# Kernel tuning notes

Hardware: AMD Instinct MI355X
Metric: run time of the kernel (lower is better)

## Reference

```python
import jax, jax.numpy as jnp
import numpy as np

B = 2
IMG = (128, 256, 256)
P = 16
E, NH, DH = 768, 12, 64
L, F = 12, 3072
WS = (512, 1024, 2048)   # LongNet segment lengths
RS = (1, 2, 4)           # matching dilation ratios
NEG = -1e9
NPATCH = (IMG[0] // P) * (IMG[1] // P) * (IMG[2] // P)
S = NPATCH + 1           # +1 CLS token


def setup_inputs() -> dict:
    key = jax.random.key(0)
    ks = jax.random.split(key, 16)
    def nrm(k, shape, std=0.02):
        return jax.random.normal(k, shape, jnp.float32) * std
    return {
        "x": jax.random.normal(ks[0], (B, 1) + IMG, jnp.float32),
        "conv_w": nrm(ks[1], (E, 1, P, P, P)),
        "conv_b": jnp.zeros((E,), jnp.float32),
        "cls_token": nrm(ks[2], (1, 1, E)),
        "pos_embed": nrm(ks[3], (1, S, E)),
        "ln1_g": jnp.ones((L, E)), "ln1_b": jnp.zeros((L, E)),
        "wq": nrm(ks[4], (L, E, E)), "bq": jnp.zeros((L, E)),
        "wk": nrm(ks[5], (L, E, E)), "bk": jnp.zeros((L, E)),
        "wv": nrm(ks[6], (L, E, E)), "bv": jnp.zeros((L, E)),
        "wo": nrm(ks[7], (L, E, E)), "bo": jnp.zeros((L, E)),
        "ln2_g": jnp.ones((L, E)), "ln2_b": jnp.zeros((L, E)),
        "w1": nrm(ks[8], (L, E, F)), "b1": jnp.zeros((L, F)),
        "w2": nrm(ks[9], (L, F, E)), "b2": jnp.zeros((L, E)),
        "normf_g": jnp.ones((E,)), "normf_b": jnp.zeros((E,)),
    }


def _ln(x, g, b, eps=1e-5):
    m = x.mean(-1, keepdims=True)
    v = ((x - m) ** 2).mean(-1, keepdims=True)
    return (x - m) * jax.lax.rsqrt(v + eps) * g + b


def _dilated_branch(q, k, v, w, r):
    # LongNet dilated attention for one (segment_length w, dilation r) config.
    # q,k,v: [B,S,H,d]. Head h uses offset h % r inside each segment of length w.
    b, s0, h, d = q.shape
    sp = -(-s0 // w) * w
    pad = sp - s0
    qp, kp, vp = (jnp.pad(t, ((0, 0), (0, pad), (0, 0), (0, 0))) for t in (q, k, v))
    n, m = sp // w, w // r
    idx = (jnp.arange(h)[:, None] % r) + jnp.arange(m)[None, :] * r      # [h,m]
    seg = lambda t: t.reshape(b, n, w, h, d).transpose(0, 1, 3, 2, 4)    # [b,n,h,w,d]
    gidx = idx[None, None, :, :, None]
    qs = jnp.take_along_axis(seg(qp), gidx, axis=3)                      # [b,n,h,m,d]
    ks = jnp.take_along_axis(seg(kp), gidx, axis=3)
    vs = jnp.take_along_axis(seg(vp), gidx, axis=3)
    kvalid = (jnp.arange(sp) < s0).reshape(n, w)[:, idx]                 # [n,h,m]
    scores = jnp.einsum('bnhqd,bnhkd->bnhqk', qs, ks) * (d ** -0.5)
    scores = jnp.where(kvalid[None, :, :, None, :], scores, NEG)
    lse = jax.nn.logsumexp(scores, axis=-1)                              # [b,n,h,m]
    out = jnp.einsum('bnhqk,bnhkd->bnhqd', jax.nn.softmax(scores, -1), vs)
    hh = jnp.arange(h)[:, None]
    out_f = jnp.zeros((b, n, h, w, d), q.dtype).at[:, :, hh, idx, :].set(out)
    lse_f = jnp.full((b, n, h, w), NEG, q.dtype).at[:, :, hh, idx].set(lse)
    return (out_f.transpose(0, 1, 3, 2, 4).reshape(b, sp, h, d),
            lse_f.transpose(0, 1, 3, 2).reshape(b, sp, h))


def _dilated_attention(q, k, v):
    # Combine branches weighted by softmax normalizers (exp lse), per LongNet.
    b, s0, h, d = q.shape
    smax = max(-(-s0 // w) * w for w in WS)
    outs, lses = [], []
    for w, r in zip(WS, RS):
        o, l = _dilated_branch(q, k, v, w, r)
        outs.append(jnp.pad(o, ((0, 0), (0, smax - o.shape[1]), (0, 0), (0, 0))))
        lses.append(jnp.pad(l, ((0, 0), (0, smax - l.shape[1]), (0, 0)),
                            constant_values=NEG))
    wgt = jax.nn.softmax(jnp.stack(lses), axis=0)[..., None]             # [nb,b,smax,h,1]
    out = (wgt * jnp.stack(outs)).sum(0)                                 # [b,smax,h,d]
    return out[:, :s0]


def reference(x, conv_w, conv_b, cls_token, pos_embed, ln1_g, ln1_b, wq, bq,
              wk, bk, wv, bv, wo, bo, ln2_g, ln2_b, w1, b1, w2, b2,
              normf_g, normf_b):
    b = x.shape[0]
    dp, hp, wp = IMG[0] // P, IMG[1] // P, IMG[2] // P
    # Conv3d patch embed with stride == kernel -> block reshape + matmul
    xp = x.reshape(b, 1, dp, P, hp, P, wp, P).transpose(0, 2, 4, 6, 1, 3, 5, 7)
    xp = xp.reshape(b, dp * hp * wp, -1) @ conv_w.reshape(E, -1).T + conv_b
    h = jnp.concatenate([jnp.broadcast_to(cls_token, (b, 1, E)), xp], axis=1)
    h = h + pos_embed  # seq length matches pos_embed, no interpolation needed

    def layer(hst, p):
        g1, lb1, Wq, Bq, Wk, Bk, Wv, Bv, Wo, Bo, g2, lb2, W1, B1, W2, B2 = p
        y = _ln(hst, g1, lb1)
        q = (y @ Wq + Bq).reshape(b, S, NH, DH)
        k = (y @ Wk + Bk).reshape(b, S, NH, DH)
        v = (y @ Wv + Bv).reshape(b, S, NH, DH)
        a = _dilated_attention(q, k, v).reshape(b, S, E) @ Wo + Bo
        hst = hst + a
        y = _ln(hst, g2, lb2)
        hst = hst + jax.nn.gelu(y @ W1 + B1, approximate=False) @ W2 + B2
        return hst, None

    params = (ln1_g, ln1_b, wq, bq, wk, bk, wv, bv, wo, bo,
              ln2_g, ln2_b, w1, b1, w2, b2)
    h, _ = jax.lax.scan(layer, h, params)
    h = _ln(h, normf_g, normf_b)
    return h[:, 0]
```

## Files before the change

kernel.cpp:

```cpp
#include <hip/hip_runtime.h>
#include <math.h>

#define SEQ 2049
#define EMB 768
#define NHEADS 12
#define QKVW 2304
#define MROWS 4098
#define MPAD 4224
#define NEGV -1000000000.0f

typedef short bs8 __attribute__((ext_vector_type(8)));
typedef float f4 __attribute__((ext_vector_type(4)));

__device__ __forceinline__ unsigned short f2bf(float f){
  union { float f; unsigned u; } x; x.f = f;
  unsigned r = x.u + 0x7fffu + ((x.u >> 16) & 1u);
  return (unsigned short)(r >> 16);
}
__device__ __forceinline__ unsigned short f2bf_fast(float f){
  union { float f; unsigned u; } x; x.f = f;
  return (unsigned short)((x.u + 0x8000u) >> 16);
}
__device__ __forceinline__ float bf2f(unsigned short u){
  union { unsigned u; float f; } x; x.u = ((unsigned)u) << 16; return x.f;
}

__device__ __forceinline__ float gelu_f(float x){
  float ax = fabsf(x)*0.70710678f;
  float t = 1.f/(1.f + 0.3275911f*ax);
  float p = t*(0.254829592f + t*(-0.284496736f + t*(1.421413741f
            + t*(-1.453152027f + t*1.061405429f))));
  float erfv = 1.f - p*__expf(-ax*ax);
  float s = (x >= 0.f) ? erfv : -erfv;
  return 0.5f*x*(1.f + s);
}

__device__ __forceinline__ void gl_lds16(const void* g, void* l){
  __builtin_amdgcn_global_load_lds((const __attribute__((address_space(1))) void*)g,
                                   (__attribute__((address_space(3))) void*)l, 16, 0, 0);
}

__global__ void wtr_k(const float* __restrict__ src, unsigned short* __restrict__ dst,
                      int K, int N, int LD, int NOFF)
{
  __shared__ float tile[32][33];
  int k0 = blockIdx.x*32, n0 = blockIdx.y*32, z = blockIdx.z;
  int tx = threadIdx.x, ty = threadIdx.y;
  const float* s = src + (size_t)z*K*N;
#pragma unroll
  for (int i=0;i<4;++i)
    tile[ty*4+i][tx] = s[(size_t)(k0+ty*4+i)*N + n0+tx];
  __syncthreads();
  unsigned short* dz = dst + ((size_t)z*LD + NOFF)*K;
#pragma unroll
  for (int i=0;i<4;++i)
    dz[(size_t)(n0+ty*4+i)*K + k0+tx] = f2bf(tile[tx][ty*4+i]);
}

__global__ void castconv_k(const float* __restrict__ src, unsigned short* __restrict__ dst){
  size_t i = ((size_t)blockIdx.x*256 + threadIdx.x)*4;
  float4 f = *(const float4*)(src+i);
  dst[i+0]=f2bf(f.x); dst[i+1]=f2bf(f.y); dst[i+2]=f2bf(f.z); dst[i+3]=f2bf(f.w);
}

__global__ void biascat_k(const float* __restrict__ bq, const float* __restrict__ bk,
                          const float* __restrict__ bv, float* __restrict__ dst){
  int i = blockIdx.x*256+threadIdx.x;
  int l = i/QKVW, c = i%QKVW;
  float v = (c<768) ? bq[l*768+c] : (c<1536 ? bk[l*768+c-768] : bv[l*768+c-1536]);
  dst[i] = v;
}

__global__ void patchify_k(const float* __restrict__ x, unsigned short* __restrict__ Xp)
{
  size_t gid = (size_t)blockIdx.x*256 + threadIdx.x;
  size_t oi = gid*4;
  int row = (int)(oi >> 12);
  int c = (int)(oi & 4095);
  int b = row >> 11; int p = row & 2047;
  int pd = p >> 8, ph = (p>>4)&15, pw = p&15;
  int pz = c >> 8, py = (c>>4)&15, px = c&15;
  size_t src = (((size_t)(b*128 + pd*16+pz)*256) + (size_t)(ph*16+py))*256 + (size_t)(pw*16+px);
  float4 f = *(const float4*)(x+src);
  Xp[oi+0]=f2bf(f.x); Xp[oi+1]=f2bf(f.y); Xp[oi+2]=f2bf(f.z); Xp[oi+3]=f2bf(f.w);
}

__global__ void assemble_k(const float* __restrict__ P, size_t pstride,
                           const float* __restrict__ cls,
                           const float* __restrict__ pos_e, float* __restrict__ H)
{
  int row = blockIdx.x; int t = threadIdx.x;
  float* hr = H + (size_t)row*EMB;
  if (row >= MROWS) { hr[t]=0.f; hr[t+256]=0.f; hr[t+512]=0.f; return; }
  int b = row / SEQ; int pos = row - b*SEQ;
#pragma unroll
  for (int c0=0;c0<3;++c0) {
    int c = t + c0*256;
    float v;
    if (pos==0) v = cls[c];
    else {
      size_t idx = ((size_t)(b*2048 + pos-1))*EMB + c;
      v = P[idx] + P[pstride+idx] + P[2*pstride+idx] + P[3*pstride+idx];
    }
    hr[c] = v + pos_e[(size_t)pos*EMB + c];
  }
}

__global__ __launch_bounds__(256) void ln_k(const float* __restrict__ H,
    const float* __restrict__ gam, const float* __restrict__ bet,
    unsigned short* __restrict__ Y)
{
  int row = blockIdx.x, t = threadIdx.x;
  const float* hr = H + (size_t)row*EMB;
  float v0 = hr[t], v1 = hr[t+256], v2 = hr[t+512];
  float s = v0+v1+v2;
#pragma unroll
  for (int off=32; off>=1; off>>=1) s += __shfl_down(s, off);
  __shared__ float r1[4], r2[4];
  if ((t&63)==0) r1[t>>6] = s;
  __syncthreads();
  float mean = (r1[0]+r1[1]+r1[2]+r1[3]) * (1.f/768.f);
  float d0=v0-mean, d1=v1-mean, d2=v2-mean;
  float q = d0*d0+d1*d1+d2*d2;
#pragma unroll
  for (int off=32; off>=1; off>>=1) q += __shfl_down(q, off);
  if ((t&63)==0) r2[t>>6] = q;
  __syncthreads();
  float rstd = rsqrtf((r2[0]+r2[1]+r2[2]+r2[3])*(1.f/768.f) + 1e-5f);
  unsigned short* yr = Y + (size_t)row*EMB;
  yr[t]     = f2bf(d0*rstd*gam[t]     + bet[t]);
  yr[t+256] = f2bf(d1*rstd*gam[t+256] + bet[t+256]);
  yr[t+512] = f2bf(d2*rstd*gam[t+512] + bet[t+512]);
}

template<int S>
__global__ __launch_bounds__(256) void ln_red_k(float* __restrict__ H,
    const float* __restrict__ P, size_t pstride,
    const float* __restrict__ gam, const float* __restrict__ bet,
    unsigned short* __restrict__ Y)
{
  int row = blockIdx.x, t = threadIdx.x;
  size_t base = (size_t)row*EMB;
  float v[3];
#pragma unroll
  for (int c0=0;c0<3;++c0) {
    size_t idx = base + t + c0*256;
    float h = H[idx];
#pragma unroll
    for (int s=0;s<S;++s) h += P[(size_t)s*pstride + idx];
    H[idx] = h; v[c0] = h;
  }
  float s = v[0]+v[1]+v[2];
#pragma unroll
  for (int off=32; off>=1; off>>=1) s += __shfl_down(s, off);
  __shared__ float r1[4], r2[4];
  if ((t&63)==0) r1[t>>6] = s;
  __syncthreads();
  float mean = (r1[0]+r1[1]+r1[2]+r1[3]) * (1.f/768.f);
  float d0=v[0]-mean, d1=v[1]-mean, d2=v[2]-mean;
  float q = d0*d0+d1*d1+d2*d2;
#pragma unroll
  for (int off=32; off>=1; off>>=1) q += __shfl_down(q, off);
  if ((t&63)==0) r2[t>>6] = q;
  __syncthreads();
  float rstd = rsqrtf((r2[0]+r2[1]+r2[2]+r2[3])*(1.f/768.f) + 1e-5f);
  unsigned short* yr = Y + base;
  yr[t]     = f2bf(d0*rstd*gam[t]     + bet[t]);
  yr[t+256] = f2bf(d1*rstd*gam[t+256] + bet[t+256]);
  yr[t+512] = f2bf(d2*rstd*gam[t+512] + bet[t+512]);
}

template<int S>
__global__ __launch_bounds__(256) void final_ln_red_k(const float* __restrict__ H,
   const float* __restrict__ P, size_t pstride,
   const float* __restrict__ gam, const float* __restrict__ bet, float* __restrict__ out)
{
  int b = blockIdx.x, t = threadIdx.x;
  size_t base = (size_t)(b*SEQ)*EMB;
  float v[3];
#pragma unroll
  for (int c0=0;c0<3;++c0) {
    size_t idx = base + t + c0*256;
    float h = H[idx];
#pragma unroll
    for (int s=0;s<S;++s) h += P[(size_t)s*pstride + idx];
    v[c0] = h;
  }
  float s = v[0]+v[1]+v[2];
#pragma unroll
  for (int off=32; off>=1; off>>=1) s += __shfl_down(s, off);
  __shared__ float r1[4], r2[4];
  if ((t&63)==0) r1[t>>6] = s;
  __syncthreads();
  float mean = (r1[0]+r1[1]+r1[2]+r1[3]) * (1.f/768.f);
  float d0=v[0]-mean, d1=v[1]-mean, d2=v[2]-mean;
  float q = d0*d0+d1*d1+d2*d2;
#pragma unroll
  for (int off=32; off>=1; off>>=1) q += __shfl_down(q, off);
  if ((t&63)==0) r2[t>>6] = q;
  __syncthreads();
  float rstd = rsqrtf((r2[0]+r2[1]+r2[2]+r2[3])*(1.f/768.f) + 1e-5f);
  out[b*EMB + t]     = d0*rstd*gam[t]     + bet[t];
  out[b*EMB + t+256] = d1*rstd*gam[t+256] + bet[t+256];
  out[b*EMB + t+512] = d2*rstd*gam[t+512] + bet[t+512];
}

template<int MODE, int NSPLIT>
__global__ __launch_bounds__(512) void gemm_k(
    const unsigned short* __restrict__ A,
    const unsigned short* __restrict__ Bt,
    const float* __restrict__ bias,
    unsigned short* __restrict__ Cb,
    float* __restrict__ Cf,
    int K, int ldc, size_t splitStride)
{
  __shared__ __attribute__((aligned(16))) unsigned short lA[3][128*32];
  __shared__ __attribute__((aligned(16))) unsigned short lB[3][128*32];
  const int tid = threadIdx.x;
  const int w = tid>>6, lane = tid&63, g = lane>>4, l16 = lane&15;
  const int lr = lane>>2;
  const int lcs = (((lane&3) ^ ((lane>>3)&3)))*8;
  const int swz = ((g ^ ((l16>>1)&3)))*8;
  const int nwg = gridDim.x*gridDim.y;
  const int id = blockIdx.y*gridDim.x + blockIdx.x;
  const int q = nwg>>3, r = nwg&7, xc = id&7, si = id>>3;
  const int nid = (xc<r ? xc*(q+1) : r*(q+1)+(xc-r)*q) + si;
  const int tm = nid / gridDim.x;
  const int tn = nid - tm*gridDim.x;
  const int kchunk = K / NSPLIT;
  const int kofs = (NSPLIT>1) ? blockIdx.z * kchunk : 0;
  const unsigned short* Ab = A + (size_t)tm*128*K + kofs;
  const unsigned short* Bb = Bt + (size_t)tn*128*K + kofs;
  const int wm = (w>>2)*64, wn = (w&3)*32;
  f4 acc[4][2] = {};
  const int nkt = kchunk>>5;

  auto STAGE = [&](int buf, int kt){
    const size_t ko = (size_t)(kt*32 + lcs);
    gl_lds16(Ab + (size_t)(w*16 + lr)*K + ko, ((char*)lA[buf]) + w*1024);
    gl_lds16(Bb + (size_t)(w*16 + lr)*K + ko, ((char*)lB[buf]) + w*1024);
  };

  STAGE(0, 0);
  STAGE(1, 1);
  for (int kt=0; kt<nkt; ++kt) {
    const int cur = kt % 3;
    if (kt+2 < nkt) {
      STAGE((kt+2)%3, kt+2);
      asm volatile("s_waitcnt vmcnt(4)" ::: "memory");
    } else if (kt+1 < nkt) {
      asm volatile("s_waitcnt vmcnt(2)" ::: "memory");
    } else {
      asm volatile("s_waitcnt vmcnt(0)" ::: "memory");
    }
    __builtin_amdgcn_sched_barrier(0);
    __builtin_amdgcn_s_barrier();
    bs8 af[4], bf[2];
#pragma unroll
    for (int mi=0;mi<4;++mi) af[mi] = *(const bs8*)(lA[cur] + (wm+mi*16+l16)*32 + swz);
#pragma unroll
    for (int ni=0;ni<2;++ni) bf[ni] = *(const bs8*)(lB[cur] + (wn+ni*16+l16)*32 + swz);
    asm volatile("s_waitcnt lgkmcnt(0)" ::: "memory");
    __builtin_amdgcn_sched_barrier(0);
    __builtin_amdgcn_s_barrier();
#pragma unroll
    for (int mi=0;mi<4;++mi)
#pragma unroll
      for (int ni=0;ni<2;++ni)
        acc[mi][ni] = __builtin_amdgcn_mfma_f32_16x16x32_bf16(af[mi], bf[ni], acc[mi][ni], 0,0,0);
  }
  const float bscale = (NSPLIT==1 || blockIdx.z==0) ? 1.f : 0.f;
#pragma unroll
  for (int mi=0;mi<4;++mi)
#pragma unroll
    for (int ni=0;ni<2;++ni) {
      int col = tn*128 + wn + ni*16 + l16;
      float bv = bias[col]*bscale;
#pragma unroll
      for (int r0=0;r0<4;++r0) {
        int row = tm*128 + wm + mi*16 + g*4 + r0;
        float val = acc[mi][ni][r0] + bv;
        if (MODE==1) val = gelu_f(val);
        if (MODE<=1) Cb[(size_t)row*ldc + col] = f2bf(val);
        else Cf[(size_t)blockIdx.z*splitStride + (size_t)row*ldc + col] = val;
      }
    }
}

__global__ __launch_bounds__(256) void attn_all_k(
    const unsigned short* __restrict__ qkv,
    unsigned short* __restrict__ O1, float* __restrict__ L1,
    unsigned short* __restrict__ O2, float* __restrict__ L2,
    unsigned short* __restrict__ O3, float* __restrict__ L3)
{
  __shared__ __attribute__((aligned(16))) unsigned short lsm[128*72 + 64*136];
  unsigned short* lK  = lsm;
  unsigned short* lVt = lsm + 128*72;
  const int tid = threadIdx.x;
  const int w = tid>>6, lane = tid&63, g = lane>>4, l16 = lane&15;

  int id = (blockIdx.x & 7)*240 + (blockIdx.x >> 3);
  int R, WSZ, NSEG; unsigned short* OB; float* LB;
  if (id < 960)       { R=1; WSZ=512;  NSEG=5; OB=O1; LB=L1; }
  else if (id < 1536) { id -= 960;  R=2; WSZ=1024; NSEG=3; OB=O2; LB=L2; }
  else                { id -= 1536; R=4; WSZ=2048; NSEG=2; OB=O3; LB=L3; }
  const int qt = id & 7; int rest = id >> 3;
  const int seg = rest % NSEG; const int bh = rest / NSEG;
  const int b = bh / NHEADS, hd = bh % NHEADS;
  const int hr = hd % R;
  const int kbase = seg*WSZ + hr;
  bs8 z = {0,0,0,0,0,0,0,0};

  if (kbase + qt*64*R >= SEQ) {
    size_t ob2 = ((size_t)(b*NSEG + seg)*NHEADS + hd)*512 + qt*64;
    int row = tid>>2, cb = (tid&3)*16;
    *(bs8*)(&OB[(ob2 + row)*64 + cb])     = z;
    *(bs8*)(&OB[(ob2 + row)*64 + cb + 8]) = z;
    if (tid < 64) LB[ob2 + tid] = NEGV;
    return;
  }
  int nvk = (SEQ - 1 - kbase)/R + 1; if (nvk > 512) nvk = 512;
  const int nck = (nvk + 127) >> 7;

  const int j0 = qt*64 + w*16;
  const unsigned short* qkvb = qkv + (size_t)b*SEQ*QKVW;

  bs8 qf0 = z, qf1 = z;
  {
    int qpos = kbase + (j0 + l16)*R;
    if (qpos < SEQ) {
      const unsigned short* qrow = qkvb + (size_t)qpos*QKVW + hd*64 + g*8;
      qf0 = *(const bs8*)(qrow);
      qf1 = *(const bs8*)(qrow + 32);
    }
  }

  const int dbK = tid&7, kkKb = tid>>3;
  const int kkV = tid&127, dbV0 = tid>>7;
  const unsigned short* pK = qkvb + (size_t)(kbase + kkKb*R)*QKVW + EMB + hd*64 + dbK*8;
  const unsigned short* pV = qkvb + (size_t)(kbase + kkV*R)*QKVW + 1536 + hd*64 + dbV0*8;
  const size_t stepIt = (size_t)32*R*QKVW;
  const size_t stepC  = (size_t)128*R*QKVW;
  int ci = 0;
  bs8 kreg[4], vreg[4];
  auto ISSUE = [&](){
    const bool full = (kbase + (ci*128 + 127)*R) < SEQ;
    if (full) {
#pragma unroll
      for (int it=0; it<4; ++it) kreg[it] = *(const bs8*)(pK + (size_t)it*stepIt);
#pragma unroll
      for (int it=0; it<4; ++it) vreg[it] = *(const bs8*)(pV + it*16);
    } else {
      const int cofs = ci*128*R;
#pragma unroll
      for (int it=0; it<4; ++it)
        kreg[it] = (kbase + (kkKb + it*32)*R + cofs < SEQ)
                   ? *(const bs8*)(pK + (size_t)it*stepIt) : z;
      const bool vv = (kbase + kkV*R + cofs) < SEQ;
#pragma unroll
      for (int it=0; it<4; ++it) vreg[it] = vv ? *(const bs8*)(pV + it*16) : z;
    }
    pK += stepC; pV += stepC; ++ci;
  };

  float rm[4], rs[4];
  f4 oacc[4] = {};
#pragma unroll
  for (int r=0;r<4;++r) { rm[r] = NEGV; rs[r] = 0.f; }

  ISSUE();
  for (int c=0; c<nck; ++c) {
    __syncthreads();
#pragma unroll
    for (int it=0; it<4; ++it) {
      *(bs8*)(lK + (kkKb + it*32)*72 + dbK*8) = kreg[it];
#pragma unroll
      for (int ii=0; ii<8; ++ii) lVt[((dbV0+it*2)*8+ii)*136 + kkV] = (unsigned short)vreg[it][ii];
    }
    __syncthreads();
    if (c+1 < nck) ISSUE();

    const bool fullc = (kbase + (c*128 + 127)*R) < SEQ;
    f4 sc[8];
    __builtin_amdgcn_s_setprio(1);
#pragma unroll
    for (int kt=0; kt<8; ++kt) {
      int key = kt*16 + l16;
      bs8 kf0 = *(const bs8*)(lK + key*72 + g*8);
      bs8 kf1 = *(const bs8*)(lK + key*72 + 32 + g*8);
      f4 acc = {0.f,0.f,0.f,0.f};
      acc = __builtin_amdgcn_mfma_f32_16x16x32_bf16(qf0, kf0, acc, 0,0,0);
      acc = __builtin_amdgcn_mfma_f32_16x16x32_bf16(qf1, kf1, acc, 0,0,0);
      sc[kt] = acc;
    }
    __builtin_amdgcn_s_setprio(0);
    __syncthreads();
    if (!fullc) {
#pragma unroll
      for (int kt=0; kt<8; ++kt) {
        bool kvld = (kbase + (c*128 + kt*16 + l16)*R) < SEQ;
#pragma unroll
        for (int r=0;r<4;++r) sc[kt][r] = kvld ? sc[kt][r] : NEGV;
      }
    }
    float scl[4];
#pragma unroll
    for (int r=0;r<4;++r) {
      float mx = sc[0][r];
#pragma unroll
      for (int kt=1;kt<8;++kt) mx = fmaxf(mx, sc[kt][r]);
      mx = fmaxf(mx, __shfl_xor(mx, 1));
      mx = fmaxf(mx, __shfl_xor(mx, 2));
      mx = fmaxf(mx, __shfl_xor(mx, 4));
      mx = fmaxf(mx, __shfl_xor(mx, 8));
      float mn = fmaxf(rm[r], mx*0.125f);
      scl[r] = __expf(rm[r] - mn);
      rm[r] = mn;
    }
#pragma unroll
    for (int r=0;r<4;++r) {
      float sm = 0.f;
      float nrm = -rm[r];
#pragma unroll
      for (int kt=0;kt<8;++kt) {
        float p = __expf(__builtin_fmaf(sc[kt][r], 0.125f, nrm));
        sc[kt][r] = p; sm += p;
      }
      rs[r] = rs[r]*scl[r] + sm;
    }
    if (scl[0]<1.f || scl[1]<1.f || scl[2]<1.f || scl[3]<1.f) {
#pragma unroll
      for (int dt=0; dt<4; ++dt)
#pragma unroll
        for (int r=0;r<4;++r) oacc[dt][r] *= scl[r];
    }
    unsigned short* Plw = lK + w*16*136;
#pragma unroll
    for (int kt=0;kt<8;++kt)
#pragma unroll
      for (int r=0;r<4;++r) {
        int row = g*4+r;
        int gr = (kt*2 + (l16>>3)) ^ ((row>>3)&1);
        Plw[row*136 + gr*8 + (l16&7)] = f2bf_fast(sc[kt][r]);
      }
    __builtin_amdgcn_s_setprio(1);
#pragma unroll
    for (int ks=0; ks<4; ++ks) {
      int grp = ((ks*4+g) ^ ((l16>>3)&1))*8;
      bs8 pa = *(const bs8*)(Plw + l16*136 + grp);
#pragma unroll
      for (int dt=0; dt<4; ++dt) {
        bs8 vb = *(const bs8*)(lVt + (dt*16+l16)*136 + ks*32 + g*8);
        oacc[dt] = __builtin_amdgcn_mfma_f32_16x16x32_bf16(pa, vb, oacc[dt], 0,0,0);
      }
    }
    __builtin_amdgcn_s_setprio(0);
  }

#pragma unroll
  for (int r=0;r<4;++r) {
    float s = rs[r];
    s += __shfl_xor(s, 1); s += __shfl_xor(s, 2);
    s += __shfl_xor(s, 4); s += __shfl_xor(s, 8);
    rs[r] = s;
  }

  size_t obase = ((size_t)(b*NSEG + seg)*NHEADS + hd)*512;
#pragma unroll
  for (int dt=0; dt<4; ++dt)
#pragma unroll
    for (int r=0;r<4;++r) {
      int j = j0 + g*4 + r;
      OB[(obase + j)*64 + dt*16 + l16] = f2bf(oacc[dt][r] / rs[r]);
    }
  if (l16 == 0) {
#pragma unroll
    for (int r=0;r<4;++r) LB[obase + j0 + g*4 + r] = rm[r] + __logf(rs[r]);
  }
}

__global__ __launch_bounds__(256) void attn_combine_k(
   const unsigned short* __restrict__ o1, const float* __restrict__ l1,
   const unsigned short* __restrict__ o2, const float* __restrict__ l2,
   const unsigned short* __restrict__ o3, const float* __restrict__ l3,
   unsigned short* __restrict__ attn)
{
  int row = blockIdx.x; int t = threadIdx.x;
  unsigned short* arow = attn + (size_t)row*EMB;
  if (row >= MROWS) { arow[t]=0; arow[t+256]=0; arow[t+512]=0; return; }
  int b = row / SEQ, pos = row - (row/SEQ)*SEQ;
#pragma unroll
  for (int c0=0; c0<3; ++c0) {
    int cc = t + c0*256;
    int hd = cc >> 6, d = cc & 63;
    float L0,L1v,L2v,O0,O1v,O2v;
    {
      int seg = pos >> 9; int j = pos & 511;
      size_t base = ((size_t)(b*5 + seg)*NHEADS + hd)*512 + j;
      L0 = l1[base]; O0 = bf2f(o1[base*64 + d]);
    }
    if ((pos & 1) == (hd & 1)) {
      int seg = pos >> 10; int j = ((pos & 1023) - (hd&1)) >> 1;
      size_t base = ((size_t)(b*3 + seg)*NHEADS + hd)*512 + j;
      L1v = l2[base]; O1v = bf2f(o2[base*64 + d]);
    } else { L1v = NEGV; O1v = 0.f; }
    if ((pos & 3) == (hd & 3)) {
      int seg = pos >> 11; int j = ((pos & 2047) - (hd&3)) >> 2;
      size_t base = ((size_t)(b*2 + seg)*NHEADS + hd)*512 + j;
      L2v = l3[base]; O2v = bf2f(o3[base*64 + d]);
    } else { L2v = NEGV; O2v = 0.f; }
    float m = fmaxf(L0, fmaxf(L1v, L2v));
    float e0 = __expf(L0-m), e1 = __expf(L1v-m), e2 = __expf(L2v-m);
    float inv = 1.f/(e0+e1+e2);
    arow[cc] = f2bf((e0*O0+e1*O1v+e2*O2v)*inv);
  }
}

extern "C" void kernel_launch(void* const* d_in, const int* in_sizes, int n_in,
                              void* d_out, int out_size, void* d_ws, size_t ws_size,
                              hipStream_t stream) {
  const float* x       = (const float*)d_in[0];
  const float* conv_w  = (const float*)d_in[1];
  const float* conv_b  = (const float*)d_in[2];
  const float* cls     = (const float*)d_in[3];
  const float* pos_e   = (const float*)d_in[4];
  const float* ln1_g   = (const float*)d_in[5];
  const float* ln1_b   = (const float*)d_in[6];
  const float* wq      = (const float*)d_in[7];
  const float* bq      = (const float*)d_in[8];
  const float* wk      = (const float*)d_in[9];
  const float* bk      = (const float*)d_in[10];
  const float* wv      = (const float*)d_in[11];
  const float* bv      = (const float*)d_in[12];
  const float* wo      = (const float*)d_in[13];
  const float* bo      = (const float*)d_in[14];
  const float* ln2_g   = (const float*)d_in[15];
  const float* ln2_b   = (const float*)d_in[16];
  const float* w1      = (const float*)d_in[17];
  const float* b1      = (const float*)d_in[18];
  const float* w2      = (const float*)d_in[19];
  const float* b2      = (const float*)d_in[20];
  const float* nf_g    = (const float*)d_in[21];
  const float* nf_b    = (const float*)d_in[22];

  char* ws = (char*)d_ws;
  size_t off = 0;
  auto alloc = [&](size_t bytes)->char* {
    char* p = ws + off; off += (bytes + 255) & ~(size_t)255; return p;
  };
  unsigned short* wqkv_t = (unsigned short*)alloc((size_t)12*2304*768*2);
  unsigned short* wo_t   = (unsigned short*)alloc((size_t)12*768*768*2);
  unsigned short* w1_t   = (unsigned short*)alloc((size_t)12*3072*768*2);
  unsigned short* w2_t   = (unsigned short*)alloc((size_t)12*768*3072*2);
  unsigned short* cw_b   = (unsigned short*)alloc((size_t)768*4096*2);
  float* bqkv            = (float*)alloc((size_t)12*2304*4);
  unsigned short* Xp     = (unsigned short*)alloc((size_t)4096*4096*2);
  float* H               = (float*)alloc((size_t)MPAD*768*4);
  float* P               = (float*)alloc((size_t)4*MPAD*768*4);
  unsigned short* Y      = (unsigned short*)alloc((size_t)MPAD*768*2);
  unsigned short* QKV    = (unsigned short*)alloc((size_t)MPAD*2304*2);
  unsigned short* ATT    = (unsigned short*)alloc((size_t)MPAD*768*2);
  unsigned short* Y2     = (unsigned short*)alloc((size_t)MPAD*3072*2);
  unsigned short* O1 = (unsigned short*)alloc((size_t)2*5*12*512*64*2);
  unsigned short* O2 = (unsigned short*)alloc((size_t)2*3*12*512*64*2);
  unsigned short* O3 = (unsigned short*)alloc((size_t)2*2*12*512*64*2);
  float* L1 = (float*)alloc((size_t)2*5*12*512*4);
  float* L2 = (float*)alloc((size_t)2*3*12*512*4);
  float* L3 = (float*)alloc((size_t)2*2*12*512*4);
  const size_t PSTR = (size_t)MPAD*768;

  dim3 tb(32,8);
  wtr_k<<<dim3(24,24,12), tb, 0, stream>>>(wq, wqkv_t, 768, 768, 2304, 0);
  wtr_k<<<dim3(24,24,12), tb, 0, stream>>>(wk, wqkv_t, 768, 768, 2304, 768);
  wtr_k<<<dim3(24,24,12), tb, 0, stream>>>(wv, wqkv_t, 768, 768, 2304, 1536);
  wtr_k<<<dim3(24,24,12), tb, 0, stream>>>(wo, wo_t, 768, 768, 768, 0);
  wtr_k<<<dim3(24,96,12), tb, 0, stream>>>(w1, w1_t, 768, 3072, 3072, 0);
  wtr_k<<<dim3(96,24,12), tb, 0, stream>>>(w2, w2_t, 3072, 768, 768, 0);
  castconv_k<<<3072,256,0,stream>>>(conv_w, cw_b);
  biascat_k<<<108,256,0,stream>>>(bq,bk,bv,bqkv);
  patchify_k<<<16384,256,0,stream>>>(x, Xp);
  gemm_k<3,4><<<dim3(6,32,4),512,0,stream>>>(Xp, cw_b, conv_b, nullptr, P, 4096, 768, PSTR);
  assemble_k<<<MPAD,256,0,stream>>>(P, PSTR, cls, pos_e, H);

  for (int l=0;l<12;++l) {
    if (l==0) ln_k<<<MPAD,256,0,stream>>>(H, ln1_g, ln1_b, Y);
    else ln_red_k<2><<<MPAD,256,0,stream>>>(H, P, PSTR, ln1_g + l*768, ln1_b + l*768, Y);
    gemm_k<0,1><<<dim3(18,33),512,0,stream>>>(Y, wqkv_t + (size_t)l*2304*768, bqkv + l*2304, QKV, nullptr, 768, 2304, 0);
    attn_all_k<<<1920,256,0,stream>>>(QKV, O1,L1,O2,L2,O3,L3);
    attn_combine_k<<<MPAD,256,0,stream>>>(O1,L1,O2,L2,O3,L3, ATT);
    gemm_k<3,2><<<dim3(6,33,2),512,0,stream>>>(ATT, wo_t + (size_t)l*768*768, bo + l*768, nullptr, P, 768, 768, PSTR);
    ln_red_k<2><<<MPAD,256,0,stream>>>(H, P, PSTR, ln2_g + l*768, ln2_b + l*768, Y);
    gemm_k<1,1><<<dim3(24,33),512,0,stream>>>(Y, w1_t + (size_t)l*3072*768, b1 + l*3072, Y2, nullptr, 768, 3072, 0);
    gemm_k<3,2><<<dim3(6,33,2),512,0,stream>>>(Y2, w2_t + (size_t)l*768*3072, b2 + l*768, nullptr, P, 3072, 768, PSTR);
  }
  final_ln_red_k<2><<<2,256,0,stream>>>(H, P, PSTR, nf_g, nf_b, (float*)d_out);
}
```

Before: 2.662 ms.

## Split attention key dimension across blocks and merge partials in combine kernel

```diff
diff --git a/kernel.cpp b/kernel.cpp
--- a/kernel.cpp
+++ b/kernel.cpp
@@ -299,7 +299,8 @@
   const int tid = threadIdx.x;
   const int w = tid>>6, lane = tid&63, g = lane>>4, l16 = lane&15;
 
-  int id = (blockIdx.x & 7)*240 + (blockIdx.x >> 3);
+  int id2 = (blockIdx.x & 7)*960 + (blockIdx.x >> 3);
+  const int ck = id2 & 3; int id = id2 >> 2;
   int R, WSZ, NSEG; unsigned short* OB; float* LB;
   if (id < 960)       { R=1; WSZ=512;  NSEG=5; OB=O1; LB=L1; }
   else if (id < 1536) { id -= 960;  R=2; WSZ=1024; NSEG=3; OB=O2; LB=L2; }
@@ -309,18 +310,18 @@
   const int b = bh / NHEADS, hd = bh % NHEADS;
   const int hr = hd % R;
   const int kbase = seg*WSZ + hr;
+  const int cofs = ck*128;
   bs8 z = {0,0,0,0,0,0,0,0};
-
-  if (kbase + qt*64*R >= SEQ) {
-    size_t ob2 = ((size_t)(b*NSEG + seg)*NHEADS + hd)*512 + qt*64;
+  size_t obase = (((size_t)(b*NSEG + seg)*NHEADS + hd)*4 + ck)*512;
+
+  if (kbase + qt*64*R >= SEQ || kbase + cofs*R >= SEQ) {
+    size_t ob2 = obase + qt*64;
     int row = tid>>2, cb = (tid&3)*16;
     *(bs8*)(&OB[(ob2 + row)*64 + cb])     = z;
     *(bs8*)(&OB[(ob2 + row)*64 + cb + 8]) = z;
     if (tid < 64) LB[ob2 + tid] = NEGV;
     return;
   }
-  int nvk = (SEQ - 1 - kbase)/R + 1; if (nvk > 512) nvk = 512;
-  const int nck = (nvk + 127) >> 7;
 
   const int j0 = qt*64 + w*16;
   const unsigned short* qkvb = qkv + (size_t)b*SEQ*QKVW;
@@ -337,125 +338,101 @@
 
   const int dbK = tid&7, kkKb = tid>>3;
   const int kkV = tid&127, dbV0 = tid>>7;
-  const unsigned short* pK = qkvb + (size_t)(kbase + kkKb*R)*QKVW + EMB + hd*64 + dbK*8;
-  const unsigned short* pV = qkvb + (size_t)(kbase + kkV*R)*QKVW + 1536 + hd*64 + dbV0*8;
+  const unsigned short* pK = qkvb + (size_t)(kbase + (cofs + kkKb)*R)*QKVW + EMB + hd*64 + dbK*8;
+  const unsigned short* pV = qkvb + (size_t)(kbase + (cofs + kkV)*R)*QKVW + 1536 + hd*64 + dbV0*8;
   const size_t stepIt = (size_t)32*R*QKVW;
-  const size_t stepC  = (size_t)128*R*QKVW;
-  int ci = 0;
+  const bool fullc = (kbase + (cofs + 127)*R) < SEQ;
   bs8 kreg[4], vreg[4];
-  auto ISSUE = [&](){
-    const bool full = (kbase + (ci*128 + 127)*R) < SEQ;
-    if (full) {
-#pragma unroll
-      for (int it=0; it<4; ++it) kreg[it] = *(const bs8*)(pK + (size_t)it*stepIt);
-#pragma unroll
-      for (int it=0; it<4; ++it) vreg[it] = *(const bs8*)(pV + it*16);
-    } else {
-      const int cofs = ci*128*R;
-#pragma unroll
-      for (int it=0; it<4; ++it)
-        kreg[it] = (kbase + (kkKb + it*32)*R + cofs < SEQ)
-                   ? *(const bs8*)(pK + (size_t)it*stepIt) : z;
-      const bool vv = (kbase + kkV*R + cofs) < SEQ;
-#pragma unroll
-      for (int it=0; it<4; ++it) vreg[it] = vv ? *(const bs8*)(pV + it*16) : z;
-    }
-    pK += stepC; pV += stepC; ++ci;
-  };
-
+  if (fullc) {
+#pragma unroll
+    for (int it=0; it<4; ++it) kreg[it] = *(const bs8*)(pK + (size_t)it*stepIt);
+#pragma unroll
+    for (int it=0; it<4; ++it) vreg[it] = *(const bs8*)(pV + it*16);
+  } else {
+#pragma unroll
+    for (int it=0; it<4; ++it)
+      kreg[it] = (kbase + (cofs + kkKb + it*32)*R < SEQ)
+                 ? *(const bs8*)(pK + (size_t)it*stepIt) : z;
+    const bool vv = (kbase + (cofs + kkV)*R) < SEQ;
+#pragma unroll
+    for (int it=0; it<4; ++it) vreg[it] = vv ? *(const bs8*)(pV + it*16) : z;
+  }
+#pragma unroll
+  for (int it=0; it<4; ++it) {
+    *(bs8*)(lK + (kkKb + it*32)*72 + dbK*8) = kreg[it];
+#pragma unroll
+    for (int ii=0; ii<8; ++ii) lVt[((dbV0+it*2)*8+ii)*136 + kkV] = (unsigned short)vreg[it][ii];
+  }
+  __syncthreads();
+
+  f4 sc[8];
+  __builtin_amdgcn_s_setprio(1);
+#pragma unroll
+  for (int kt=0; kt<8; ++kt) {
+    int key = kt*16 + l16;
+    bs8 kf0 = *(const bs8*)(lK + key*72 + g*8);
+    bs8 kf1 = *(const bs8*)(lK + key*72 + 32 + g*8);
+    f4 acc = {0.f,0.f,0.f,0.f};
+    acc = __builtin_amdgcn_mfma_f32_16x16x32_bf16(qf0, kf0, acc, 0,0,0);
+    acc = __builtin_amdgcn_mfma_f32_16x16x32_bf16(qf1, kf1, acc, 0,0,0);
+    sc[kt] = acc;
+  }
+  __builtin_amdgcn_s_setprio(0);
+  __syncthreads();
+
+  if (!fullc) {
+#pragma unroll
+    for (int kt=0; kt<8; ++kt) {
+      bool kvld = (kbase + (cofs + kt*16 + l16)*R) < SEQ;
+#pragma unroll
+      for (int r=0;r<4;++r) sc[kt][r] = kvld ? sc[kt][r] : NEGV;
+    }
+  }
   float rm[4], rs[4];
+#pragma unroll
+  for (int r=0;r<4;++r) {
+    float mx = sc[0][r];
+#pragma unroll
+    for (int kt=1;kt<8;++kt) mx = fmaxf(mx, sc[kt][r]);
+    mx = fmaxf(mx, __shfl_xor(mx, 1));
+    mx = fmaxf(mx, __shfl_xor(mx, 2));
+    mx = fmaxf(mx, __shfl_xor(mx, 4));
+    mx = fmaxf(mx, __shfl_xor(mx, 8));
+    rm[r] = mx*0.125f;
+  }
+#pragma unroll
+  for (int r=0;r<4;++r) {
+    float sm = 0.f;
+    float nrm = -rm[r];
+#pragma unroll
+    for (int kt=0;kt<8;++kt) {
+      float p = __expf(__builtin_fmaf(sc[kt][r], 0.125f, nrm));
+      sc[kt][r] = p; sm += p;
+    }
+    rs[r] = sm;
+  }
+  unsigned short* Plw = lK + w*16*136;
+#pragma unroll
+  for (int kt=0;kt<8;++kt)
+#pragma unroll
+    for (int r=0;r<4;++r) {
+      int row = g*4+r;
+      int gr = (kt*2 + (l16>>3)) ^ ((row>>3)&1);
+      Plw[row*136 + gr*8 + (l16&7)] = f2bf_fast(sc[kt][r]);
+    }
   f4 oacc[4] = {};
-#pragma unroll
-  for (int r=0;r<4;++r) { rm[r] = NEGV; rs[r] = 0.f; }
-
-  ISSUE();
-  for (int c=0; c<nck; ++c) {
-    __syncthreads();
-#pragma unroll
-    for (int it=0; it<4; ++it) {
-      *(bs8*)(lK + (kkKb + it*32)*72 + dbK*8) = kreg[it];
-#pragma unroll
-      for (int ii=0; ii<8; ++ii) lVt[((dbV0+it*2)*8+ii)*136 + kkV] = (unsigned short)vreg[it][ii];
-    }
-    __syncthreads();
-    if (c+1 < nck) ISSUE();
-
-    const bool fullc = (kbase + (c*128 + 127)*R) < SEQ;
-    f4 sc[8];
-    __builtin_amdgcn_s_setprio(1);
-#pragma unroll
-    for (int kt=0; kt<8; ++kt) {
-      int key = kt*16 + l16;
-      bs8 kf0 = *(const bs8*)(lK + key*72 + g*8);
-      bs8 kf1 = *(const bs8*)(lK + key*72 + 32 + g*8);
-      f4 acc = {0.f,0.f,0.f,0.f};
-      acc = __builtin_amdgcn_mfma_f32_16x16x32_bf16(qf0, kf0, acc, 0,0,0);
-      acc = __builtin_amdgcn_mfma_f32_16x16x32_bf16(qf1, kf1, acc, 0,0,0);
-      sc[kt] = acc;
-    }
-    __builtin_amdgcn_s_setprio(0);
-    __syncthreads();
-    if (!fullc) {
-#pragma unroll
-      for (int kt=0; kt<8; ++kt) {
-        bool kvld = (kbase + (c*128 + kt*16 + l16)*R) < SEQ;
-#pragma unroll
-        for (int r=0;r<4;++r) sc[kt][r] = kvld ? sc[kt][r] : NEGV;
-      }
-    }
-    float scl[4];
-#pragma unroll
-    for (int r=0;r<4;++r) {
-      float mx = sc[0][r];
-#pragma unroll
-      for (int kt=1;kt<8;++kt) mx = fmaxf(mx, sc[kt][r]);
-      mx = fmaxf(mx, __shfl_xor(mx, 1));
-      mx = fmaxf(mx, __shfl_xor(mx, 2));
-      mx = fmaxf(mx, __shfl_xor(mx, 4));
-      mx = fmaxf(mx, __shfl_xor(mx, 8));
-      float mn = fmaxf(rm[r], mx*0.125f);
-      scl[r] = __expf(rm[r] - mn);
-      rm[r] = mn;
-    }
-#pragma unroll
-    for (int r=0;r<4;++r) {
-      float sm = 0.f;
-      float nrm = -rm[r];
-#pragma unroll
-      for (int kt=0;kt<8;++kt) {
-        float p = __expf(__builtin_fmaf(sc[kt][r], 0.125f, nrm));
-        sc[kt][r] = p; sm += p;
-      }
-      rs[r] = rs[r]*scl[r] + sm;
-    }
-    if (scl[0]<1.f || scl[1]<1.f || scl[2]<1.f || scl[3]<1.f) {
-#pragma unroll
-      for (int dt=0; dt<4; ++dt)
-#pragma unroll
-        for (int r=0;r<4;++r) oacc[dt][r] *= scl[r];
-    }
-    unsigned short* Plw = lK + w*16*136;
-#pragma unroll
-    for (int kt=0;kt<8;++kt)
-#pragma unroll
-      for (int r=0;r<4;++r) {
-        int row = g*4+r;
-        int gr = (kt*2 + (l16>>3)) ^ ((row>>3)&1);
-        Plw[row*136 + gr*8 + (l16&7)] = f2bf_fast(sc[kt][r]);
-      }
-    __builtin_amdgcn_s_setprio(1);
-#pragma unroll
-    for (int ks=0; ks<4; ++ks) {
-      int grp = ((ks*4+g) ^ ((l16>>3)&1))*8;
-      bs8 pa = *(const bs8*)(Plw + l16*136 + grp);
-#pragma unroll
-      for (int dt=0; dt<4; ++dt) {
-        bs8 vb = *(const bs8*)(lVt + (dt*16+l16)*136 + ks*32 + g*8);
-        oacc[dt] = __builtin_amdgcn_mfma_f32_16x16x32_bf16(pa, vb, oacc[dt], 0,0,0);
-      }
-    }
-    __builtin_amdgcn_s_setprio(0);
-  }
+  __builtin_amdgcn_s_setprio(1);
+#pragma unroll
+  for (int ks=0; ks<4; ++ks) {
+    int grp = ((ks*4+g) ^ ((l16>>3)&1))*8;
+    bs8 pa = *(const bs8*)(Plw + l16*136 + grp);
+#pragma unroll
+    for (int dt=0; dt<4; ++dt) {
+      bs8 vb = *(const bs8*)(lVt + (dt*16+l16)*136 + ks*32 + g*8);
+      oacc[dt] = __builtin_amdgcn_mfma_f32_16x16x32_bf16(pa, vb, oacc[dt], 0,0,0);
+    }
+  }
+  __builtin_amdgcn_s_setprio(0);
 
 #pragma unroll
   for (int r=0;r<4;++r) {
@@ -465,7 +442,6 @@
     rs[r] = s;
   }
 
-  size_t obase = ((size_t)(b*NSEG + seg)*NHEADS + hd)*512;
 #pragma unroll
   for (int dt=0; dt<4; ++dt)
 #pragma unroll
@@ -493,26 +469,50 @@
   for (int c0=0; c0<3; ++c0) {
     int cc = t + c0*256;
     int hd = cc >> 6, d = cc & 63;
-    float L0,L1v,L2v,O0,O1v,O2v;
+    float La[12], Oa[12];
     {
       int seg = pos >> 9; int j = pos & 511;
-      size_t base = ((size_t)(b*5 + seg)*NHEADS + hd)*512 + j;
-      L0 = l1[base]; O0 = bf2f(o1[base*64 + d]);
+      size_t base0 = (((size_t)(b*5 + seg)*NHEADS + hd)*4)*512 + j;
+#pragma unroll
+      for (int ck=0;ck<4;++ck) {
+        La[ck] = l1[base0 + ck*512];
+        Oa[ck] = bf2f(o1[(base0 + ck*512)*64 + d]);
+      }
     }
     if ((pos & 1) == (hd & 1)) {
       int seg = pos >> 10; int j = ((pos & 1023) - (hd&1)) >> 1;
-      size_t base = ((size_t)(b*3 + seg)*NHEADS + hd)*512 + j;
-      L1v = l2[base]; O1v = bf2f(o2[base*64 + d]);
-    } else { L1v = NEGV; O1v = 0.f; }
+      size_t base0 = (((size_t)(b*3 + seg)*NHEADS + hd)*4)*512 + j;
+#pragma unroll
+      for (int ck=0;ck<4;++ck) {
+        La[4+ck] = l2[base0 + ck*512];
+        Oa[4+ck] = bf2f(o2[(base0 + ck*512)*64 + d]);
+      }
+    } else {
+#pragma unroll
+      for (int ck=0;ck<4;++ck) { La[4+ck] = NEGV; Oa[4+ck] = 0.f; }
+    }
     if ((pos & 3) == (hd & 3)) {
       int seg = pos >> 11; int j = ((pos & 2047) - (hd&3)) >> 2;
-      size_t base = ((size_t)(b*2 + seg)*NHEADS + hd)*512 + j;
-      L2v = l3[base]; O2v = bf2f(o3[base*64 + d]);
-    } else { L2v = NEGV; O2v = 0.f; }
-    float m = fmaxf(L0, fmaxf(L1v, L2v));
-    float e0 = __expf(L0-m), e1 = __expf(L1v-m), e2 = __expf(L2v-m);
-    float inv = 1.f/(e0+e1+e2);
-    arow[cc] = f2bf((e0*O0+e1*O1v+e2*O2v)*inv);
+      size_t base0 = (((size_t)(b*2 + seg)*NHEADS + hd)*4)*512 + j;
+#pragma unroll
+      for (int ck=0;ck<4;++ck) {
+        La[8+ck] = l3[base0 + ck*512];
+        Oa[8+ck] = bf2f(o3[(base0 + ck*512)*64 + d]);
+      }
+    } else {
+#pragma unroll
+      for (int ck=0;ck<4;++ck) { La[8+ck] = NEGV; Oa[8+ck] = 0.f; }
+    }
+    float M = La[0];
+#pragma unroll
+    for (int i=1;i<12;++i) M = fmaxf(M, La[i]);
+    float acc = 0.f, wsum = 0.f;
+#pragma unroll
+    for (int i=0;i<12;++i) {
+      float e = __expf(La[i] - M);
+      acc += e * Oa[i]; wsum += e;
+    }
+    arow[cc] = f2bf(acc / wsum);
   }
 }
 
@@ -561,12 +561,12 @@
   unsigned short* QKV    = (unsigned short*)alloc((size_t)MPAD*2304*2);
   unsigned short* ATT    = (unsigned short*)alloc((size_t)MPAD*768*2);
   unsigned short* Y2     = (unsigned short*)alloc((size_t)MPAD*3072*2);
-  unsigned short* O1 = (unsigned short*)alloc((size_t)2*5*12*512*64*2);
-  unsigned short* O2 = (unsigned short*)alloc((size_t)2*3*12*512*64*2);
-  unsigned short* O3 = (unsigned short*)alloc((size_t)2*2*12*512*64*2);
-  float* L1 = (float*)alloc((size_t)2*5*12*512*4);
-  float* L2 = (float*)alloc((size_t)2*3*12*512*4);
-  float* L3 = (float*)alloc((size_t)2*2*12*512*4);
+  unsigned short* O1 = (unsigned short*)alloc((size_t)2*5*12*4*512*64*2);
+  unsigned short* O2 = (unsigned short*)alloc((size_t)2*3*12*4*512*64*2);
+  unsigned short* O3 = (unsigned short*)alloc((size_t)2*2*12*4*512*64*2);
+  float* L1 = (float*)alloc((size_t)2*5*12*4*512*4);
+  float* L2 = (float*)alloc((size_t)2*3*12*4*512*4);
+  float* L3 = (float*)alloc((size_t)2*2*12*4*512*4);
   const size_t PSTR = (size_t)MPAD*768;
 
   dim3 tb(32,8);
@@ -586,7 +586,7 @@
     if (l==0) ln_k<<<MPAD,256,0,stream>>>(H, ln1_g, ln1_b, Y);
     else ln_red_k<2><<<MPAD,256,0,stream>>>(H, P, PSTR, ln1_g + l*768, ln1_b + l*768, Y);
     gemm_k<0,1><<<dim3(18,33),512,0,stream>>>(Y, wqkv_t + (size_t)l*2304*768, bqkv + l*2304, QKV, nullptr, 768, 2304, 0);
-    attn_all_k<<<1920,256,0,stream>>>(QKV, O1,L1,O2,L2,O3,L3);
+    attn_all_k<<<7680,256,0,stream>>>(QKV, O1,L1,O2,L2,O3,L3);
     attn_combine_k<<<MPAD,256,0,stream>>>(O1,L1,O2,L2,O3,L3, ATT);
     gemm_k<3,2><<<dim3(6,33,2),512,0,stream>>>(ATT, wo_t + (size_t)l*768*768, bo + l*768, nullptr, P, 768, 768, PSTR);
     ln_red_k<2><<<MPAD,256,0,stream>>>(H, P, PSTR, ln2_g + l*768, ln2_b + l*768, Y);
```

Result: no change. 2.654 ms (-0.3%).
